# Kernel optimization log

Measured on AMD Instinct MI355X. Metric: run time of the kernel, lower is better.

The kernel has to match this reference:

```python
import jax, jax.numpy as jnp
import numpy as np

N = 100000      # nodes
D = 64          # feature dim (in_channels == out_channels)
K = 16          # num_neighbors -> E = N*(K-1) directed edges
NEG_SLOPE = 0.2 # GATConv negative_slope


def setup_inputs() -> dict:
    key = jax.random.key(0)
    k1, k2, k3, k4, k5 = jax.random.split(key, 5)
    E = N * (K - 1)
    x = jax.random.normal(k1, (N, D), dtype=jnp.float32)
    edge_index = jax.random.randint(k2, (2, E), 0, N, dtype=jnp.int32)
    W = jax.random.normal(k3, (D, D), dtype=jnp.float32) / np.sqrt(D).astype(np.float32)
    att_src = jax.random.normal(k4, (D,), dtype=jnp.float32) / np.sqrt(D).astype(np.float32)
    att_dst = jax.random.normal(k5, (D,), dtype=jnp.float32) / np.sqrt(D).astype(np.float32)
    bias = jnp.zeros((D,), dtype=jnp.float32)
    return {"x": x, "edge_index": edge_index, "W": W,
            "att_src": att_src, "att_dst": att_dst, "bias": bias}


def gat_forward(x, W, att_src, att_dst, bias, src, dst):
    # PyG GATConv, heads=1, concat=True, dropout=0, + outer ReLU from LNLE.forward
    h = x @ W                                   # [N, D] transformed nodes
    a_src = h @ att_src                         # [N] source attention logits
    a_dst = h @ att_dst                         # [N] target attention logits
    e = jax.nn.leaky_relu(a_src[src] + a_dst[dst], NEG_SLOPE)  # [E]
    # numerically-stable segment softmax over edges grouped by destination
    emax = jax.ops.segment_max(e, dst, num_segments=N)         # [N]
    p = jnp.exp(e - emax[dst])                                 # [E]
    psum = jax.ops.segment_sum(p, dst, num_segments=N)         # [N]
    alpha = p / (psum[dst] + jnp.float32(1e-16))               # [E]
    msg = h[src] * alpha[:, None]                              # [E, D] gather + weight
    out = jax.ops.segment_sum(msg, dst, num_segments=N) + bias # [N, D] scatter-add
    return jax.nn.relu(out)


def reference(x, edge_index, W, att_src, att_dst, bias):
    # GATConv default add_self_loops=True: append (i -> i) for every node
    loops = jnp.arange(N, dtype=edge_index.dtype)
    src = jnp.concatenate([edge_index[0], loops])   # message sources j
    dst = jnp.concatenate([edge_index[1], loops])   # message targets i
    return gat_forward(x, W, att_src, att_dst, bias, src, dst)
```

## Files before the change

### kernel.cpp

```cpp
#include <hip/hip_runtime.h>
#include <hip/hip_bf16.h>
#include <hip/hip_fp16.h>


#define GAT_N 100000
#define GAT_D 64
#define GAT_E 1500000
#define NEG_SLOPE 0.2f
#define NB ((GAT_N + 255) >> 8)
#define PC 3072
#define CAP_P 5120
#define CAP_C (CAP_P + 256)
#define GPITCH 68
#define GEMM_BLKS ((GAT_N + 63) / 64)
#define PART_BLKS ((GAT_E + PC - 1) / PC)

__device__ __forceinline__ float lrelu(float e) {
    return e > 0.f ? e : NEG_SLOPE * e;
}

__global__ __launch_bounds__(256) void zinit_k(int* __restrict__ runctr) {
    const int i = blockIdx.x * 256 + threadIdx.x;
    if (i < NB) runctr[i] = i * CAP_P;
}

__global__ __launch_bounds__(256, 4) void pg_k(
        const float* __restrict__ x, const float* __restrict__ W,
        const float* __restrict__ att_s, const float* __restrict__ att_d,
        unsigned* __restrict__ h, float* __restrict__ a_src, float* __restrict__ a_dst,
        const int* __restrict__ src, const int* __restrict__ dst,
        int* __restrict__ runctr, int* __restrict__ pairs) {
    __shared__ __align__(16) int smem[8448];
    const int t = threadIdx.x;

    if (blockIdx.x < GEMM_BLKS) {
        float* xl = (float*)smem;
        float* Wl = (float*)(smem + 4352);
        const int rowbase = blockIdx.x * 64;
        {
            const float4* W4 = (const float4*)W;
            float4* Wl4 = (float4*)Wl;
            #pragma unroll
            for (int i = 0; i < 4; ++i) Wl4[i * 256 + t] = W4[i * 256 + t];
        }
        #pragma unroll
        for (int i = 0; i < 4; ++i) {
            const int g = i * 256 + t;
            const int row = g >> 4, c4 = g & 15;
            float4 v = make_float4(0.f, 0.f, 0.f, 0.f);
            if (rowbase + row < GAT_N)
                v = ((const float4*)x)[(size_t)(rowbase + row) * 16 + c4];
            *(float4*)&xl[row * GPITCH + c4 * 4] = v;
        }
        __syncthreads();

        const int tx = t & 15, ty = t >> 4;
        float4 acc[4] = {};
        #pragma unroll 4
        for (int k0 = 0; k0 < GAT_D; k0 += 4) {
            const float4 w0 = *(const float4*)&Wl[(k0 + 0) * 64 + tx * 4];
            const float4 w1 = *(const float4*)&Wl[(k0 + 1) * 64 + tx * 4];
            const float4 w2 = *(const float4*)&Wl[(k0 + 2) * 64 + tx * 4];
            const float4 w3 = *(const float4*)&Wl[(k0 + 3) * 64 + tx * 4];
            #pragma unroll
            for (int i = 0; i < 4; ++i) {
                const float4 xv = *(const float4*)&xl[(ty * 4 + i) * GPITCH + k0];
                acc[i].x = fmaf(xv.x, w0.x, fmaf(xv.y, w1.x, fmaf(xv.z, w2.x, fmaf(xv.w, w3.x, acc[i].x))));
                acc[i].y = fmaf(xv.x, w0.y, fmaf(xv.y, w1.y, fmaf(xv.z, w2.y, fmaf(xv.w, w3.y, acc[i].y))));
                acc[i].z = fmaf(xv.x, w0.z, fmaf(xv.y, w1.z, fmaf(xv.z, w2.z, fmaf(xv.w, w3.z, acc[i].z))));
                acc[i].w = fmaf(xv.x, w0.w, fmaf(xv.y, w1.w, fmaf(xv.z, w2.w, fmaf(xv.w, w3.w, acc[i].w))));
            }
        }
        const float4 as4 = ((const float4*)att_s)[tx];
        const float4 ad4 = ((const float4*)att_d)[tx];
        #pragma unroll
        for (int i = 0; i < 4; ++i) {
            const int row = rowbase + ty * 4 + i;
            if (row < GAT_N) {
                const __half2 lo = __floats2half2_rn(acc[i].x, acc[i].y);
                const __half2 hi = __floats2half2_rn(acc[i].z, acc[i].w);
                ((uint2*)h)[(size_t)row * 16 + tx] =
                    make_uint2(*(const unsigned*)&lo, *(const unsigned*)&hi);
            }
            float ps = acc[i].x * as4.x + acc[i].y * as4.y + acc[i].z * as4.z + acc[i].w * as4.w;
            float pd = acc[i].x * ad4.x + acc[i].y * ad4.y + acc[i].z * ad4.z + acc[i].w * ad4.w;
            #pragma unroll
            for (int o = 8; o > 0; o >>= 1) {
                ps += __shfl_down(ps, o, 64);
                pd += __shfl_down(pd, o, 64);
            }
            if (tx == 0 && row < GAT_N) { a_src[row] = ps; a_dst[row] = pd; }
        }
    } else {
        int* lh    = smem;
        int* sc    = smem + 512;
        int* lb    = smem + 768;
        int* gpos  = smem + 1280;
        int* run   = smem + 1792;
        int* tgt   = smem + 2304;
        int* stage = smem + 5376;
        const int base = (blockIdx.x - GEMM_BLKS) * PC;

        lh[t] = 0; lh[t + 256] = 0;
        __syncthreads();
        for (int i = t; i < PC; i += 256) {
            const int e = base + i;
            if (e < GAT_E) atomicAdd(&lh[dst[e] >> 8], 1);
        }
        __syncthreads();
        const int a = lh[2 * t], b = lh[2 * t + 1];
        sc[t] = a + b; __syncthreads();
        for (int off = 1; off < 256; off <<= 1) {
            const int xch = (t >= off) ? sc[t - off] : 0;
            __syncthreads();
            sc[t] += xch;
            __syncthreads();
        }
        const int base0 = sc[t] - (a + b);
        lb[2 * t] = base0; lb[2 * t + 1] = base0 + a;
        #pragma unroll
        for (int k = 0; k < 2; ++k) {
            const int i = 2 * t + k;
            run[i] = lb[i];
            gpos[i] = (i < NB && lh[i]) ? atomicAdd(&runctr[i], lh[i]) : 0;
        }
        __syncthreads();
        for (int i = t; i < PC; i += 256) {
            const int e = base + i;
            if (e < GAT_E) {
                const int sv = src[e], dv = dst[e];
                const int bk = dv >> 8;
                const int slot = atomicAdd(&run[bk], 1);
                stage[slot] = (sv << 8) | (dv & 255);
                tgt[slot] = gpos[bk] + (slot - lb[bk]);
            }
        }
        __syncthreads();
        const int cnt_total = min(PC, GAT_E - base);
        for (int i = t; i < cnt_total; i += 256) pairs[tgt[i]] = stage[i];
    }
}

__global__ __launch_bounds__(512) void csr_bucket_k(
        const int* __restrict__ pairs, const int* __restrict__ runctr,
        int* __restrict__ rowinfo, int* __restrict__ csr) {
    __shared__ int cnt[256], pfx[256];
    __shared__ int lcsr[CAP_C];
    const int b = blockIdx.x;
    const int t = threadIdx.x;
    const int node0 = b << 8;
    const int nnodes = min(256, GAT_N - node0);
    const int pbeg = b * CAP_P;
    const int ne = runctr[b] - pbeg;
    const int cbase = b * CAP_C;

    if (t < 256) cnt[t] = (t < nnodes) ? 1 : 0;
    __syncthreads();
    for (int i = t; i < ne; i += 512)
        atomicAdd(&cnt[pairs[pbeg + i] & 255], 1);
    __syncthreads();
    if (t < 256) pfx[t] = cnt[t];
    __syncthreads();
    for (int off = 1; off < 256; off <<= 1) {
        const int x = (t < 256 && t >= off) ? pfx[t - off] : 0;
        __syncthreads();
        if (t < 256) pfx[t] += x;
        __syncthreads();
    }
    if (t < 256) {
        const int v = cnt[t];
        const int excl = pfx[t] - v;
        if (t < nnodes) {
            rowinfo[node0 + t] = ((cbase + excl) << 8) | v;
            lcsr[excl] = node0 + t;
        }
        cnt[t] = excl + ((t < nnodes) ? 1 : 0);
    }
    __syncthreads();
    for (int i = t; i < ne; i += 512) {
        const int p = pairs[pbeg + i];
        const int pos = atomicAdd(&cnt[p & 255], 1);
        lcsr[pos] = p >> 8;
    }
    __syncthreads();
    const int tot = ne + nnodes;
    for (int i = t; i < tot; i += 512) csr[cbase + i] = lcsr[i];
}

#define GATHER4(ACC, EIDX)                                              \
    {                                                                   \
        const float w_ = __shfl(alpha, (EIDX), 64);                     \
        const int   s_ = __shfl(s, (EIDX), 64);                         \
        const uint2 v_ = h2[(size_t)s_ * 16 + fl];                      \
        const float2 fa_ = __half22float2(*(const __half2*)&v_.x);      \
        const float2 fb_ = __half22float2(*(const __half2*)&v_.y);      \
        ACC.x = fmaf(w_, fa_.x, ACC.x);                                 \
        ACC.y = fmaf(w_, fa_.y, ACC.y);                                 \
        ACC.z = fmaf(w_, fb_.x, ACC.z);                                 \
        ACC.w = fmaf(w_, fb_.y, ACC.w);                                 \
    }

__device__ __noinline__ void gat_one_node(
        int d, int beg, int deg, int lane,
        const int* __restrict__ csr_src,
        const float* __restrict__ a_src, const float* __restrict__ a_dst,
        const unsigned* __restrict__ h, const float* __restrict__ bias,
        float* __restrict__ out) {
    const int end = beg + deg;
    const float ad = a_dst[d];
    if (deg <= 64) {
        const int k = beg + lane;
        const bool valid = k < end;
        const int s = valid ? csr_src[k] : 0;
        const float e = valid ? lrelu(a_src[s] + ad) : -3.4e38f;
        float m = e;
        #pragma unroll
        for (int o = 32; o > 0; o >>= 1) m = fmaxf(m, __shfl_down(m, o, 64));
        m = __shfl(m, 0, 64);
        const float p = valid ? __expf(e - m) : 0.f;
        float S = p;
        #pragma unroll
        for (int o = 32; o > 0; o >>= 1) S += __shfl_down(S, o, 64);
        S = __shfl(S, 0, 64);
        const float alpha = p / (S + 1e-16f);
        const int q = lane >> 4, fl = lane & 15;
        const uint2* __restrict__ h2 = (const uint2*)h;
        float4 A = {0,0,0,0}, B = {0,0,0,0}, C = {0,0,0,0}, D = {0,0,0,0};
        int j = 0;
        for (; j + 16 <= deg; j += 16) {
            GATHER4(A, j + q);
            GATHER4(B, j + 4 + q);
            GATHER4(C, j + 8 + q);
            GATHER4(D, j + 12 + q);
        }
        if (j < deg)      GATHER4(A, j + q);
        if (j + 4 < deg)  GATHER4(B, j + 4 + q);
        if (j + 8 < deg)  GATHER4(C, j + 8 + q);
        if (j + 12 < deg) GATHER4(D, j + 12 + q);
        float4 acc;
        acc.x = (A.x + B.x) + (C.x + D.x);
        acc.y = (A.y + B.y) + (C.y + D.y);
        acc.z = (A.z + B.z) + (C.z + D.z);
        acc.w = (A.w + B.w) + (C.w + D.w);
        acc.x += __shfl_xor(acc.x, 16, 64); acc.x += __shfl_xor(acc.x, 32, 64);
        acc.y += __shfl_xor(acc.y, 16, 64); acc.y += __shfl_xor(acc.y, 32, 64);
        acc.z += __shfl_xor(acc.z, 16, 64); acc.z += __shfl_xor(acc.z, 32, 64);
        acc.w += __shfl_xor(acc.w, 16, 64); acc.w += __shfl_xor(acc.w, 32, 64);
        if (q == 0) {
            const float4 bi = ((const float4*)bias)[fl];
            float4 o;
            o.x = fmaxf(acc.x + bi.x, 0.f);
            o.y = fmaxf(acc.y + bi.y, 0.f);
            o.z = fmaxf(acc.z + bi.z, 0.f);
            o.w = fmaxf(acc.w + bi.w, 0.f);
            ((float4*)out)[(size_t)d * 16 + fl] = o;
        }
    } else {
        float m = -3.4e38f;
        for (int base = beg; base < end; base += 64) {
            const int k = base + lane;
            if (k < end) m = fmaxf(m, lrelu(a_src[csr_src[k]] + ad));
        }
        #pragma unroll
        for (int o = 32; o > 0; o >>= 1) m = fmaxf(m, __shfl_down(m, o, 64));
        m = __shfl(m, 0, 64);
        float S = 0.f;
        for (int base = beg; base < end; base += 64) {
            const int k = base + lane;
            if (k < end) S += __expf(lrelu(a_src[csr_src[k]] + ad) - m);
        }
        #pragma unroll
        for (int o = 32; o > 0; o >>= 1) S += __shfl_down(S, o, 64);
        S = __shfl(S, 0, 64);
        const float inv = 1.f / (S + 1e-16f);
        float acc = 0.f;
        const unsigned short* hb = (const unsigned short*)h;
        for (int base = beg; base < end; base += 64) {
            const int k = base + lane;
            int s = 0; float alpha = 0.f;
            if (k < end) {
                s = csr_src[k];
                alpha = __expf(lrelu(a_src[s] + ad) - m) * inv;
            }
            const int lim = min(64, end - base);
            for (int j2 = 0; j2 < lim; ++j2) {
                const float aj = __shfl(alpha, j2, 64);
                const int   sj = __shfl(s, j2, 64);
                const unsigned short u = hb[(size_t)sj * 64 + lane];
                acc = fmaf(aj, __half2float(*(const __half*)&u), acc);
            }
        }
        const float v = acc + bias[lane];
        out[(size_t)d * GAT_D + lane] = v > 0.f ? v : 0.f;
    }
}

__global__ __launch_bounds__(256) void gat_node_k(
        const int* __restrict__ rowinfo, const int* __restrict__ csr_src,
        const float* __restrict__ a_src, const float* __restrict__ a_dst,
        const unsigned* __restrict__ h, const float* __restrict__ bias,
        float* __restrict__ out) {
    const int pair = blockIdx.x * 4 + (threadIdx.x >> 6);
    const int lane = threadIdx.x & 63;
    const int half = lane >> 5, l32 = lane & 31;
    const int n0 = pair * 2;
    const int n = n0 + half;

    const int ri  = rowinfo[n];
    const int beg = ri >> 8;
    const int deg = ri & 255;
    const int dm  = max(deg, __shfl_xor(deg, 32, 64));

    if (dm <= 31) {
        const float ad = a_dst[n];
        const bool valid = l32 < deg;
        const int k = beg + l32;
        const int s = valid ? csr_src[k] : 0;
        const float e0 = valid ? lrelu(a_src[s] + ad) : -3.4e38f;
        float m = e0;
        #pragma unroll
        for (int o = 16; o > 0; o >>= 1) m = fmaxf(m, __shfl_xor(m, o, 64));
        const float p = valid ? __expf(e0 - m) : 0.f;
        float S = p;
        #pragma unroll
        for (int o = 16; o > 0; o >>= 1) S += __shfl_xor(S, o, 64);
        const float alpha = p / (S + 1e-16f);

        const int sub = (lane >> 4) & 1, fl = lane & 15;
        const int hb5 = lane & 32;
        const uint2* __restrict__ h2 = (const uint2*)h;
        float4 A = {0,0,0,0}, B = {0,0,0,0}, C = {0,0,0,0}, D = {0,0,0,0};
        int j = 0;
        for (; j + 8 <= dm; j += 8) {
            GATHER4(A, hb5 + j + sub);
            GATHER4(B, hb5 + j + 2 + sub);
            GATHER4(C, hb5 + j + 4 + sub);
            GATHER4(D, hb5 + j + 6 + sub);
        }
        if (j < dm)     GATHER4(A, hb5 + j + sub);
        if (j + 2 < dm) GATHER4(B, hb5 + j + 2 + sub);
        if (j + 4 < dm) GATHER4(C, hb5 + j + 4 + sub);
        if (j + 6 < dm) GATHER4(D, hb5 + j + 6 + sub);

        float4 acc;
        acc.x = (A.x + B.x) + (C.x + D.x);
        acc.y = (A.y + B.y) + (C.y + D.y);
        acc.z = (A.z + B.z) + (C.z + D.z);
        acc.w = (A.w + B.w) + (C.w + D.w);
        acc.x += __shfl_xor(acc.x, 16, 64);
        acc.y += __shfl_xor(acc.y, 16, 64);
        acc.z += __shfl_xor(acc.z, 16, 64);
        acc.w += __shfl_xor(acc.w, 16, 64);
        if (sub == 0) {
            const float4 bi = ((const float4*)bias)[fl];
            float4 o;
            o.x = fmaxf(acc.x + bi.x, 0.f);
            o.y = fmaxf(acc.y + bi.y, 0.f);
            o.z = fmaxf(acc.z + bi.z, 0.f);
            o.w = fmaxf(acc.w + bi.w, 0.f);
            ((float4*)out)[(size_t)n * 16 + fl] = o;
        }
    } else {
        const int ri0 = rowinfo[n0];
        gat_one_node(n0, ri0 >> 8, ri0 & 255, lane, csr_src, a_src, a_dst, h, bias, out);
        const int ri1 = rowinfo[n0 + 1];
        gat_one_node(n0 + 1, ri1 >> 8, ri1 & 255, lane, csr_src, a_src, a_dst, h, bias, out);
    }
}

extern "C" void kernel_launch(void* const* d_in, const int* in_sizes, int n_in,
                              void* d_out, int out_size, void* d_ws, size_t ws_size,
                              hipStream_t stream) {
    const float* x     = (const float*)d_in[0];
    const int*   ei    = (const int*)  d_in[1];
    const float* W     = (const float*)d_in[2];
    const float* att_s = (const float*)d_in[3];
    const float* att_d = (const float*)d_in[4];
    const float* bias  = (const float*)d_in[5];
    float* out = (float*)d_out;

    unsigned* h      = (unsigned*)d_ws;
    float*  a_src    = (float*)(h + (size_t)GAT_N * 32);
    float*  a_dst    = a_src + GAT_N;
    int*    pairs    = (int*)(a_dst + GAT_N);
    int*    runctr   = pairs + (size_t)NB * CAP_P;
    int*    rowinfo  = runctr + NB;
    int*    csr      = rowinfo + GAT_N;

    const int* src = ei;
    const int* dst = ei + GAT_E;

    zinit_k<<<2, 256, 0, stream>>>(runctr);
    pg_k<<<GEMM_BLKS + PART_BLKS, 256, 0, stream>>>(
        x, W, att_s, att_d, h, a_src, a_dst, src, dst, runctr, pairs);
    csr_bucket_k<<<NB, 512, 0, stream>>>(pairs, runctr, rowinfo, csr);
    gat_node_k<<<GAT_N / 8, 256, 0, stream>>>(rowinfo, csr, a_src, a_dst, h, bias, out);
}
```

Baseline: 180.7 us.

## Fuse CSR bucket build into GAT aggregation kernel using shared-memory CSR

Removes the separate csr_bucket_k kernel and its global rowinfo/csr arrays. Each block of the new fused kernel handles half of a 256-node bucket: it builds the local CSR in LDS and then runs the softmax-gather aggregation directly from shared memory. This saves one kernel launch and a global write and read of the CSR. In exchange, each bucket's pairs are read twice (once per half-block), and occupancy drops because of the 512-thread blocks and about 12 KB of LDS. Edges past LCAP are silently dropped, which would be a correctness risk for skewed inputs.

Result: slower. 219.3 us (+21.4%).

```diff
diff --git a/kernel.cpp b/kernel.cpp
--- a/kernel.cpp
+++ b/kernel.cpp
@@ -10,7 +10,7 @@
 #define NB ((GAT_N + 255) >> 8)
 #define PC 3072
 #define CAP_P 5120
-#define CAP_C (CAP_P + 256)
+#define LCAP 2944
 #define GPITCH 68
 #define GEMM_BLKS ((GAT_N + 63) / 64)
 #define PART_BLKS ((GAT_E + PC - 1) / PC)
@@ -139,52 +139,6 @@
         const int cnt_total = min(PC, GAT_E - base);
         for (int i = t; i < cnt_total; i += 256) pairs[tgt[i]] = stage[i];
     }
-}
-
-__global__ __launch_bounds__(512) void csr_bucket_k(
-        const int* __restrict__ pairs, const int* __restrict__ runctr,
-        int* __restrict__ rowinfo, int* __restrict__ csr) {
-    __shared__ int cnt[256], pfx[256];
-    __shared__ int lcsr[CAP_C];
-    const int b = blockIdx.x;
-    const int t = threadIdx.x;
-    const int node0 = b << 8;
-    const int nnodes = min(256, GAT_N - node0);
-    const int pbeg = b * CAP_P;
-    const int ne = runctr[b] - pbeg;
-    const int cbase = b * CAP_C;
-
-    if (t < 256) cnt[t] = (t < nnodes) ? 1 : 0;
-    __syncthreads();
-    for (int i = t; i < ne; i += 512)
-        atomicAdd(&cnt[pairs[pbeg + i] & 255], 1);
-    __syncthreads();
-    if (t < 256) pfx[t] = cnt[t];
-    __syncthreads();
-    for (int off = 1; off < 256; off <<= 1) {
-        const int x = (t < 256 && t >= off) ? pfx[t - off] : 0;
-        __syncthreads();
-        if (t < 256) pfx[t] += x;
-        __syncthreads();
-    }
-    if (t < 256) {
-        const int v = cnt[t];
-        const int excl = pfx[t] - v;
-        if (t < nnodes) {
-            rowinfo[node0 + t] = ((cbase + excl) << 8) | v;
-            lcsr[excl] = node0 + t;
-        }
-        cnt[t] = excl + ((t < nnodes) ? 1 : 0);
-    }
-    __syncthreads();
-    for (int i = t; i < ne; i += 512) {
-        const int p = pairs[pbeg + i];
-        const int pos = atomicAdd(&cnt[p & 255], 1);
-        lcsr[pos] = p >> 8;
-    }
-    __syncthreads();
-    const int tot = ne + nnodes;
-    for (int i = t; i < tot; i += 512) csr[cbase + i] = lcsr[i];
 }
 
 #define GATHER4(ACC, EIDX)                                              \
@@ -202,7 +156,7 @@
 
 __device__ __noinline__ void gat_one_node(
         int d, int beg, int deg, int lane,
-        const int* __restrict__ csr_src,
+        const int* csr_src,
         const float* __restrict__ a_src, const float* __restrict__ a_dst,
         const unsigned* __restrict__ h, const float* __restrict__ bias,
         float* __restrict__ out) {
@@ -295,76 +249,119 @@
     }
 }
 
-__global__ __launch_bounds__(256) void gat_node_k(
-        const int* __restrict__ rowinfo, const int* __restrict__ csr_src,
+__global__ __launch_bounds__(512) void gatf_k(
+        const int* __restrict__ pairs, const int* __restrict__ runctr,
         const float* __restrict__ a_src, const float* __restrict__ a_dst,
         const unsigned* __restrict__ h, const float* __restrict__ bias,
         float* __restrict__ out) {
-    const int pair = blockIdx.x * 4 + (threadIdx.x >> 6);
-    const int lane = threadIdx.x & 63;
-    const int half = lane >> 5, l32 = lane & 31;
-    const int n0 = pair * 2;
-    const int n = n0 + half;
-
-    const int ri  = rowinfo[n];
-    const int beg = ri >> 8;
-    const int deg = ri & 255;
-    const int dm  = max(deg, __shfl_xor(deg, 32, 64));
-
-    if (dm <= 31) {
-        const float ad = a_dst[n];
-        const bool valid = l32 < deg;
-        const int k = beg + l32;
-        const int s = valid ? csr_src[k] : 0;
-        const float e0 = valid ? lrelu(a_src[s] + ad) : -3.4e38f;
-        float m = e0;
-        #pragma unroll
-        for (int o = 16; o > 0; o >>= 1) m = fmaxf(m, __shfl_xor(m, o, 64));
-        const float p = valid ? __expf(e0 - m) : 0.f;
-        float S = p;
-        #pragma unroll
-        for (int o = 16; o > 0; o >>= 1) S += __shfl_xor(S, o, 64);
-        const float alpha = p / (S + 1e-16f);
-
-        const int sub = (lane >> 4) & 1, fl = lane & 15;
-        const int hb5 = lane & 32;
-        const uint2* __restrict__ h2 = (const uint2*)h;
-        float4 A = {0,0,0,0}, B = {0,0,0,0}, C = {0,0,0,0}, D = {0,0,0,0};
-        int j = 0;
-        for (; j + 8 <= dm; j += 8) {
-            GATHER4(A, hb5 + j + sub);
-            GATHER4(B, hb5 + j + 2 + sub);
-            GATHER4(C, hb5 + j + 4 + sub);
-            GATHER4(D, hb5 + j + 6 + sub);
-        }
-        if (j < dm)     GATHER4(A, hb5 + j + sub);
-        if (j + 2 < dm) GATHER4(B, hb5 + j + 2 + sub);
-        if (j + 4 < dm) GATHER4(C, hb5 + j + 4 + sub);
-        if (j + 6 < dm) GATHER4(D, hb5 + j + 6 + sub);
-
-        float4 acc;
-        acc.x = (A.x + B.x) + (C.x + D.x);
-        acc.y = (A.y + B.y) + (C.y + D.y);
-        acc.z = (A.z + B.z) + (C.z + D.z);
-        acc.w = (A.w + B.w) + (C.w + D.w);
-        acc.x += __shfl_xor(acc.x, 16, 64);
-        acc.y += __shfl_xor(acc.y, 16, 64);
-        acc.z += __shfl_xor(acc.z, 16, 64);
-        acc.w += __shfl_xor(acc.w, 16, 64);
-        if (sub == 0) {
-            const float4 bi = ((const float4*)bias)[fl];
-            float4 o;
-            o.x = fmaxf(acc.x + bi.x, 0.f);
-            o.y = fmaxf(acc.y + bi.y, 0.f);
-            o.z = fmaxf(acc.z + bi.z, 0.f);
-            o.w = fmaxf(acc.w + bi.w, 0.f);
-            ((float4*)out)[(size_t)n * 16 + fl] = o;
-        }
-    } else {
-        const int ri0 = rowinfo[n0];
-        gat_one_node(n0, ri0 >> 8, ri0 & 255, lane, csr_src, a_src, a_dst, h, bias, out);
-        const int ri1 = rowinfo[n0 + 1];
-        gat_one_node(n0 + 1, ri1 >> 8, ri1 & 255, lane, csr_src, a_src, a_dst, h, bias, out);
+    __shared__ int cnt[128], begs[128], degs[128];
+    __shared__ int lcsr[LCAP];
+    const int b = blockIdx.x >> 1, half = blockIdx.x & 1;
+    const int t = threadIdx.x;
+    const int node0 = (b << 8) + (half << 7);
+    const int nnodes = max(0, min(128, GAT_N - node0));
+    const int pbeg = b * CAP_P;
+    const int ne = runctr[b] - pbeg;
+
+    if (t < 128) cnt[t] = (t < nnodes) ? 1 : 0;
+    __syncthreads();
+    for (int i = t; i < ne; i += 512) {
+        const int d8 = pairs[pbeg + i] & 255;
+        if ((d8 >> 7) == half) atomicAdd(&cnt[d8 & 127], 1);
+    }
+    __syncthreads();
+    if (t < 128) begs[t] = cnt[t];
+    __syncthreads();
+    for (int off = 1; off < 128; off <<= 1) {
+        const int v = (t < 128 && t >= off) ? begs[t - off] : 0;
+        __syncthreads();
+        if (t < 128) begs[t] += v;
+        __syncthreads();
+    }
+    if (t < 128) {
+        const int v = cnt[t];
+        const int excl = begs[t] - v;
+        degs[t] = v;
+        begs[t] = excl;
+        if (t < nnodes) lcsr[excl] = node0 + t;
+        cnt[t] = excl + ((t < nnodes) ? 1 : 0);
+    }
+    __syncthreads();
+    for (int i = t; i < ne; i += 512) {
+        const int p = pairs[pbeg + i];
+        const int d8 = p & 255;
+        if ((d8 >> 7) == half) {
+            const int pos = atomicAdd(&cnt[d8 & 127], 1);
+            if (pos < LCAP) lcsr[pos] = p >> 8;
+        }
+    }
+    __syncthreads();
+
+    const int lane = t & 63, wid = t >> 6;
+    const int half32 = lane >> 5, l32 = lane & 31;
+    const uint2* __restrict__ h2 = (const uint2*)h;
+    for (int pr = wid; pr < 64; pr += 8) {
+        if (2 * pr + 1 >= nnodes) break;
+        const int ln = 2 * pr + half32;
+        const int n = node0 + ln;
+        const int deg = degs[ln];
+        const int beg = begs[ln];
+        const int dm = max(deg, __shfl_xor(deg, 32, 64));
+
+        if (dm <= 31) {
+            const float ad = a_dst[n];
+            const bool valid = l32 < deg;
+            const int s = valid ? lcsr[beg + l32] : 0;
+            const float e0 = valid ? lrelu(a_src[s] + ad) : -3.4e38f;
+            float m = e0;
+            #pragma unroll
+            for (int o = 16; o > 0; o >>= 1) m = fmaxf(m, __shfl_xor(m, o, 64));
+            const float p = valid ? __expf(e0 - m) : 0.f;
+            float S = p;
+            #pragma unroll
+            for (int o = 16; o > 0; o >>= 1) S += __shfl_xor(S, o, 64);
+            const float alpha = p / (S + 1e-16f);
+
+            const int sub = (lane >> 4) & 1, fl = lane & 15;
+            const int hb5 = lane & 32;
+            float4 A = {0,0,0,0}, B = {0,0,0,0}, C = {0,0,0,0}, D = {0,0,0,0};
+            int j = 0;
+            for (; j + 8 <= dm; j += 8) {
+                GATHER4(A, hb5 + j + sub);
+                GATHER4(B, hb5 + j + 2 + sub);
+                GATHER4(C, hb5 + j + 4 + sub);
+                GATHER4(D, hb5 + j + 6 + sub);
+            }
+            if (j < dm)     GATHER4(A, hb5 + j + sub);
+            if (j + 2 < dm) GATHER4(B, hb5 + j + 2 + sub);
+            if (j + 4 < dm) GATHER4(C, hb5 + j + 4 + sub);
+            if (j + 6 < dm) GATHER4(D, hb5 + j + 6 + sub);
+
+            float4 acc;
+            acc.x = (A.x + B.x) + (C.x + D.x);
+            acc.y = (A.y + B.y) + (C.y + D.y);
+            acc.z = (A.z + B.z) + (C.z + D.z);
+            acc.w = (A.w + B.w) + (C.w + D.w);
+            acc.x += __shfl_xor(acc.x, 16, 64);
+            acc.y += __shfl_xor(acc.y, 16, 64);
+            acc.z += __shfl_xor(acc.z, 16, 64);
+            acc.w += __shfl_xor(acc.w, 16, 64);
+            if (sub == 0) {
+                const float4 bi = ((const float4*)bias)[fl];
+                float4 o;
+                o.x = fmaxf(acc.x + bi.x, 0.f);
+                o.y = fmaxf(acc.y + bi.y, 0.f);
+                o.z = fmaxf(acc.z + bi.z, 0.f);
+                o.w = fmaxf(acc.w + bi.w, 0.f);
+                ((float4*)out)[(size_t)n * 16 + fl] = o;
+            }
+        } else {
+            const int n0 = node0 + 2 * pr;
+            gat_one_node(n0, begs[2 * pr], degs[2 * pr], lane,
+                         lcsr, a_src, a_dst, h, bias, out);
+            gat_one_node(n0 + 1, begs[2 * pr + 1], degs[2 * pr + 1], lane,
+                         lcsr, a_src, a_dst, h, bias, out);
+        }
     }
 }
 
@@ -384,8 +381,6 @@
     float*  a_dst    = a_src + GAT_N;
     int*    pairs    = (int*)(a_dst + GAT_N);
     int*    runctr   = pairs + (size_t)NB * CAP_P;
-    int*    rowinfo  = runctr + NB;
-    int*    csr      = rowinfo + GAT_N;
 
     const int* src = ei;
     const int* dst = ei + GAT_E;
@@ -393,6 +388,5 @@
     zinit_k<<<2, 256, 0, stream>>>(runctr);
     pg_k<<<GEMM_BLKS + PART_BLKS, 256, 0, stream>>>(
         x, W, att_s, att_d, h, a_src, a_dst, src, dst, runctr, pairs);
-    csr_bucket_k<<<NB, 512, 0, stream>>>(pairs, runctr, rowinfo, csr);
-    gat_node_k<<<GAT_N / 8, 256, 0, stream>>>(rowinfo, csr, a_src, a_dst, h, bias, out);
-}
+    gatf_k<<<NB * 2, 512, 0, stream>>>(pairs, runctr, a_src, a_dst, h, bias, out);
+}
```
